# Performance work log

Measured on AMD Instinct MI355X. Metric: run time of the kernel, lower is better.

The kernel has to match this reference:

```python
import jax, jax.numpy as jnp
import numpy as np

B, S, D_IN, D_H = 4, 2048, 1024, 1024

def setup_inputs() -> dict:
    key = jax.random.key(0)
    kx, kq, kk, kv = jax.random.split(key, 4)
    # nn.Linear default init: U(-1/sqrt(fan_in), 1/sqrt(fan_in)); stored as [out, in]
    bound = 1.0 / np.sqrt(D_IN)
    x = jax.random.normal(kx, (B, S, D_IN), dtype=jnp.float32)
    W_q = jax.random.uniform(kq, (D_H, D_IN), jnp.float32, -bound, bound)
    W_k = jax.random.uniform(kk, (D_H, D_IN), jnp.float32, -bound, bound)
    W_v = jax.random.uniform(kv, (D_H, D_IN), jnp.float32, -bound, bound)
    return {"x": x, "W_q": W_q, "W_k": W_k, "W_v": W_v}

def reference(x, W_q, W_k, W_v):
    # Q = x @ W_q.T, etc. (nn.Linear with bias=False)
    Q = jnp.einsum('bsd,hd->bsh', x, W_q)
    K = jnp.einsum('bsd,hd->bsh', x, W_k)
    V = jnp.einsum('bsd,hd->bsh', x, W_v)
    # NOTE: original scales by sqrt(Q.shape[1]) == sqrt(seq_len), not sqrt(d)
    scale = 1.0 / jnp.sqrt(jnp.asarray(Q.shape[1], Q.dtype))
    scores = jnp.einsum('bqh,bkh->bqk', Q, K) * scale  # [B,S,S]
    attn = jax.nn.softmax(scores, axis=-1)
    return jnp.einsum('bqk,bkh->bqh', attn, V)
```

## Files before the change

kernel.cpp:

```cpp
#include <hip/hip_runtime.h>

typedef unsigned short ushort_t;
typedef __attribute__((ext_vector_type(8))) __bf16 bf16x8;
typedef __attribute__((ext_vector_type(4))) float floatx4;

__device__ __forceinline__ ushort_t f2bf(float f) {
    unsigned int u = __builtin_bit_cast(unsigned int, f);
    u = (u + 0x7fffu + ((u >> 16) & 1u)) >> 16;
    return (ushort_t)u;
}

__device__ __forceinline__ void async16(const ushort_t* g, ushort_t* l) {
    __builtin_amdgcn_global_load_lds(
        (const __attribute__((address_space(1))) unsigned int*)g,
        (__attribute__((address_space(3))) unsigned int*)l,
        16 , 0 , 0 );
}

__device__ __forceinline__ int sw(int row, int cg) {
    return ((row << 2) + ((cg ^ row ^ (row >> 2)) & 3)) << 3;
}

__device__ __forceinline__ int xcd_swz(int bid, int cpx) {
    return (bid & 7) * cpx + (bid >> 3);
}

template <int N>
__device__ __forceinline__ void vwait() {
    if constexpr (N == 0)      asm volatile("s_waitcnt vmcnt(0)" ::: "memory");
    else if constexpr (N == 3) asm volatile("s_waitcnt vmcnt(3)" ::: "memory");
    else if constexpr (N == 4) asm volatile("s_waitcnt vmcnt(4)" ::: "memory");
    else if constexpr (N == 6) asm volatile("s_waitcnt vmcnt(6)" ::: "memory");
    else if constexpr (N == 8) asm volatile("s_waitcnt vmcnt(8)" ::: "memory");
    else static_assert(N == 0, "unsupported vmcnt");
}

template <int BM, int BN, int IM, int IN, int NW, int NS>
__device__ __forceinline__ void gemm_core_p(
    const ushort_t* __restrict__ A, int lda,
    const ushort_t* __restrict__ B, int ldb,
    int K, int tile_m, int tile_n,
    ushort_t* buf,
    floatx4 (&acc)[IM][IN]) {

    constexpr int NT = NW * 64;
    constexpr int SA = BM * 4 / NT;
    constexpr int SB = BN * 4 / NT;
    constexpr int Q  = SA + SB;
    constexpr int SLOT = (BM + BN) * 32;
    constexpr int BOFF = BM * 32;

    const int tid  = threadIdx.x;
    const int lane = tid & 63;
    const int wave = tid >> 6;
    const int wm   = wave >> 1, wn = wave & 1;
    const int quad = lane >> 4;
    const int l16  = lane & 15;

#pragma unroll
    for (int i = 0; i < IM; i++)
#pragma unroll
        for (int j = 0; j < IN; j++) acc[i][j] = (floatx4){0.f, 0.f, 0.f, 0.f};

    const ushort_t* ga[SA];
    int la[SA];
#pragma unroll
    for (int s = 0; s < SA; s++) {
        int seg = tid + s * NT;
        int r = seg >> 2, c = (seg ^ r ^ (r >> 2)) & 3;
        ga[s] = A + (long)(r + tile_m) * lda + c * 8;
        la[s] = seg * 8;
    }
    const ushort_t* gb[SB];
    int lb[SB];
#pragma unroll
    for (int s = 0; s < SB; s++) {
        int seg = tid + s * NT;
        int r = seg >> 2, c = (seg ^ r ^ (r >> 2)) & 3;
        gb[s] = B + (long)(r + tile_n) * ldb + c * 8;
        lb[s] = BOFF + seg * 8;
    }

    const int nk = K >> 5;

#pragma unroll
    for (int p = 0; p < NS - 1; ++p) {
#pragma unroll
        for (int s = 0; s < SA; s++) async16(ga[s] + p * 32, buf + p * SLOT + la[s]);
#pragma unroll
        for (int s = 0; s < SB; s++) async16(gb[s] + p * 32, buf + p * SLOT + lb[s]);
    }

    int slot = 0, slot2 = NS - 1;
    for (int k = 0; k < nk; ++k) {
        const int rem = nk - 1 - k;
        if (rem >= NS - 2) {
            vwait<(NS - 2) * Q>();
        } else if (NS >= 4 && rem == 1) {
            vwait<Q>();
        } else {
            vwait<0>();
        }
        __builtin_amdgcn_s_barrier();
        asm volatile("" ::: "memory");

        if (k + NS - 1 < nk) {
            const int koff = (k + NS - 1) << 5;
            ushort_t* dst = buf + slot2 * SLOT;
#pragma unroll
            for (int s = 0; s < SA; s++) async16(ga[s] + koff, dst + la[s]);
#pragma unroll
            for (int s = 0; s < SB; s++) async16(gb[s] + koff, dst + lb[s]);
        }

        const ushort_t* as = buf + slot * SLOT;
        const ushort_t* bs = as + BOFF;
        bf16x8 af[IM], bfr[IN];
#pragma unroll
        for (int im = 0; im < IM; im++)
            af[im] = *(const bf16x8*)&as[sw(wm * IM * 16 + im * 16 + l16, quad)];
#pragma unroll
        for (int in = 0; in < IN; in++)
            bfr[in] = *(const bf16x8*)&bs[sw(wn * IN * 16 + in * 16 + l16, quad)];
#pragma unroll
        for (int im = 0; im < IM; im++)
#pragma unroll
            for (int in = 0; in < IN; in++)
                acc[im][in] = __builtin_amdgcn_mfma_f32_16x16x32_bf16(
                    af[im], bfr[in], acc[im][in], 0, 0, 0);

        slot  = (slot == NS - 1) ? 0 : slot + 1;
        slot2 = (slot2 == NS - 1) ? 0 : slot2 + 1;
    }
}

template <int MODE>
__device__ __forceinline__ void tile256_body(
    const ushort_t* __restrict__ sb,
    ushort_t* __restrict__ ldn,
    ushort_t* __restrict__ ldc,
    const ushort_t* __restrict__ gA, const ushort_t* __restrict__ gB,
    int lda, int ldb, int t,
    int rb0, int rb1, int abase, int bbase,
    floatx4 (&acc)[8][4]) {

    bf16x8 aR[4][2], bKc[2][2], bCc[2][2];

#pragma unroll
    for (int fr = 0; fr < 4; fr++) {
        aR[fr][0] = *(const bf16x8*)&sb[abase + fr * 1024 + rb0];
        aR[fr][1] = *(const bf16x8*)&sb[abase + fr * 1024 + rb1];
    }
#pragma unroll
    for (int fc = 0; fc < 2; fc++) {
        bKc[fc][0] = *(const bf16x8*)&sb[bbase + fc * 1024 + rb0];
        bKc[fc][1] = *(const bf16x8*)&sb[bbase + fc * 1024 + rb1];
    }
    if constexpr (MODE <= 1) {
        async16(gA + (long)128 * lda + (long)(t + 1) * 64, ldn + 8192);
        async16(gA + (long)192 * lda + (long)(t + 1) * 64, ldn + 12288);
    }
    asm volatile("s_waitcnt lgkmcnt(8)");
    __builtin_amdgcn_s_barrier();
    asm volatile("s_waitcnt lgkmcnt(0)");
    __builtin_amdgcn_s_setprio(1);
#pragma unroll
    for (int fr = 0; fr < 4; fr++)
#pragma unroll
        for (int fc = 0; fc < 2; fc++) {
            acc[fr][fc] = __builtin_amdgcn_mfma_f32_16x16x32_bf16(
                aR[fr][0], bKc[fc][0], acc[fr][fc], 0, 0, 0);
            acc[fr][fc] = __builtin_amdgcn_mfma_f32_16x16x32_bf16(
                aR[fr][1], bKc[fc][1], acc[fr][fc], 0, 0, 0);
        }
    __builtin_amdgcn_s_setprio(0);
    __builtin_amdgcn_s_barrier();

#pragma unroll
    for (int fc = 0; fc < 2; fc++) {
        bCc[fc][0] = *(const bf16x8*)&sb[bbase + (fc + 2) * 1024 + rb0];
        bCc[fc][1] = *(const bf16x8*)&sb[bbase + (fc + 2) * 1024 + rb1];
    }
    __builtin_amdgcn_s_barrier();
    asm volatile("s_waitcnt lgkmcnt(0)");
    __builtin_amdgcn_s_setprio(1);
#pragma unroll
    for (int fr = 0; fr < 4; fr++)
#pragma unroll
        for (int fc = 0; fc < 2; fc++) {
            acc[fr][fc + 2] = __builtin_amdgcn_mfma_f32_16x16x32_bf16(
                aR[fr][0], bCc[fc][0], acc[fr][fc + 2], 0, 0, 0);
            acc[fr][fc + 2] = __builtin_amdgcn_mfma_f32_16x16x32_bf16(
                aR[fr][1], bCc[fc][1], acc[fr][fc + 2], 0, 0, 0);
        }
    __builtin_amdgcn_s_setprio(0);
    __builtin_amdgcn_s_barrier();

#pragma unroll
    for (int fr = 0; fr < 4; fr++) {
        aR[fr][0] = *(const bf16x8*)&sb[abase + (fr + 4) * 1024 + rb0];
        aR[fr][1] = *(const bf16x8*)&sb[abase + (fr + 4) * 1024 + rb1];
    }
    if constexpr (MODE == 0) {
        async16(gB + (long)(t + 2) * 64,                  ldc + 16384);
        async16(gB + (long)64 * ldb + (long)(t + 2) * 64, ldc + 20480);
    }
    __builtin_amdgcn_s_barrier();
    asm volatile("s_waitcnt lgkmcnt(0)");
    __builtin_amdgcn_s_setprio(1);
#pragma unroll
    for (int fr = 0; fr < 4; fr++)
#pragma unroll
        for (int fc = 0; fc < 2; fc++) {
            acc[fr + 4][fc + 2] = __builtin_amdgcn_mfma_f32_16x16x32_bf16(
                aR[fr][0], bCc[fc][0], acc[fr + 4][fc + 2], 0, 0, 0);
            acc[fr + 4][fc + 2] = __builtin_amdgcn_mfma_f32_16x16x32_bf16(
                aR[fr][1], bCc[fc][1], acc[fr + 4][fc + 2], 0, 0, 0);
        }
    __builtin_amdgcn_s_setprio(0);
    __builtin_amdgcn_s_barrier();

    if constexpr (MODE == 0) {
        async16(gB + (long)128 * ldb + (long)(t + 2) * 64, ldc + 24576);
        async16(gB + (long)192 * ldb + (long)(t + 2) * 64, ldc + 28672);
        async16(gA + (long)(t + 2) * 64,                   ldc);
        async16(gA + (long)64 * lda + (long)(t + 2) * 64,  ldc + 4096);
    }
    __builtin_amdgcn_s_barrier();
    __builtin_amdgcn_s_setprio(1);
#pragma unroll
    for (int fr = 0; fr < 4; fr++)
#pragma unroll
        for (int fc = 0; fc < 2; fc++) {
            acc[fr + 4][fc] = __builtin_amdgcn_mfma_f32_16x16x32_bf16(
                aR[fr][0], bKc[fc][0], acc[fr + 4][fc], 0, 0, 0);
            acc[fr + 4][fc] = __builtin_amdgcn_mfma_f32_16x16x32_bf16(
                aR[fr][1], bKc[fc][1], acc[fr + 4][fc], 0, 0, 0);
        }
    __builtin_amdgcn_s_setprio(0);
    if constexpr (MODE == 0) asm volatile("s_waitcnt vmcnt(6)");
    else if constexpr (MODE == 1) asm volatile("s_waitcnt vmcnt(0)");
    __builtin_amdgcn_s_barrier();
}

__device__ __forceinline__ void gemm256_8ph(
    const ushort_t* __restrict__ A, int lda,
    const ushort_t* __restrict__ B, int ldb,
    int K, int tile_m, int tile_n,
    ushort_t* buf,
    floatx4 (&acc)[8][4]) {

    const int tid  = threadIdx.x;
    const int lane = tid & 63;
    const int wave = tid >> 6;
    const int wm   = wave >> 2;
    const int wn   = wave & 3;
    const int quad = lane >> 4;
    const int l16  = lane & 15;

#pragma unroll
    for (int i = 0; i < 8; i++)
#pragma unroll
        for (int j = 0; j < 4; j++) acc[i][j] = (floatx4){0.f, 0.f, 0.f, 0.f};

    const int srow = tid >> 3;
    const int scg  = (tid & 7) ^ (srow & 7);
    const ushort_t* gA = A + (long)(tile_m + srow) * lda + scg * 8;
    const ushort_t* gB = B + (long)(tile_n + srow) * ldb + scg * 8;
    ushort_t* const ld = buf + tid * 8;

    const int rb0 = l16 * 64 + (((quad)     ^ (l16 & 7)) << 3);
    const int rb1 = l16 * 64 + (((quad + 4) ^ (l16 & 7)) << 3);
    const int abase = wm * 8192;
    const int bbase = 16384 + (wn >> 1) * 8192 + (wn & 1) * 4096;

    const int nt = K >> 6;

    async16(gA,                    ld);
    async16(gA + (long)64 * lda,   ld + 4096);
    async16(gB,                    ld + 16384);
    async16(gB + (long)64 * ldb,   ld + 20480);
    async16(gB + (long)128 * ldb,  ld + 24576);
    async16(gB + (long)192 * ldb,  ld + 28672);
    async16(gA + (long)128 * lda,  ld + 8192);
    async16(gA + (long)192 * lda,  ld + 12288);
    async16(gB + 64,                   ld + 32768 + 16384);
    async16(gB + (long)64 * ldb + 64,  ld + 32768 + 20480);
    async16(gB + (long)128 * ldb + 64, ld + 32768 + 24576);
    async16(gB + (long)192 * ldb + 64, ld + 32768 + 28672);
    async16(gA + 64,                   ld + 32768);
    async16(gA + (long)64 * lda + 64,  ld + 32768 + 4096);
    asm volatile("s_waitcnt vmcnt(6)");
    __builtin_amdgcn_s_barrier();

    int t = 0;
#pragma unroll 1
    for (; t < nt - 2; ++t) {
        const int p = t & 1;
        tile256_body<0>(buf + p * 32768, ld + (p ^ 1) * 32768, ld + p * 32768,
                        gA, gB, lda, ldb, t, rb0, rb1, abase, bbase, acc);
    }
    {
        const int p = t & 1;
        tile256_body<1>(buf + p * 32768, ld + (p ^ 1) * 32768, ld + p * 32768,
                        gA, gB, lda, ldb, t, rb0, rb1, abase, bbase, acc);
        ++t;
    }
    {
        const int p = t & 1;
        tile256_body<2>(buf + p * 32768, ld + (p ^ 1) * 32768, ld + p * 32768,
                        gA, gB, lda, ldb, t, rb0, rb1, abase, bbase, acc);
    }
}

template <int MODE>
__device__ __forceinline__ void tile_bn256_body(
    const ushort_t* __restrict__ sb,
    ushort_t* __restrict__ ldn,
    ushort_t* __restrict__ ldc,
    const ushort_t* __restrict__ gA, const ushort_t* __restrict__ gB,
    int lda, int ldb, int t,
    int rb0, int rb1, int ab, int bb,
    floatx4 (&acc)[4][4]) {

    bf16x8 aR[4][2], bKc[2][2], bCc[2][2];

#pragma unroll
    for (int fr = 0; fr < 4; fr++) {
        aR[fr][0] = *(const bf16x8*)&sb[ab + fr * 1024 + rb0];
        aR[fr][1] = *(const bf16x8*)&sb[ab + fr * 1024 + rb1];
    }
#pragma unroll
    for (int fc = 0; fc < 2; fc++) {
        bKc[fc][0] = *(const bf16x8*)&sb[bb + fc * 4096 + rb0];
        bKc[fc][1] = *(const bf16x8*)&sb[bb + fc * 4096 + rb1];
    }
    if constexpr (MODE <= 1) {
        async16(gB + (long)128 * ldb + (long)(t + 1) * 64, ldn + 16384);
        async16(gB + (long)192 * ldb + (long)(t + 1) * 64, ldn + 20480);
    }
    asm volatile("s_waitcnt lgkmcnt(8)");
    __builtin_amdgcn_s_barrier();
    asm volatile("s_waitcnt lgkmcnt(0)");
    __builtin_amdgcn_s_setprio(1);
#pragma unroll
    for (int fr = 0; fr < 4; fr++)
#pragma unroll
        for (int fc = 0; fc < 2; fc++) {
            acc[fr][fc] = __builtin_amdgcn_mfma_f32_16x16x32_bf16(
                aR[fr][0], bKc[fc][0], acc[fr][fc], 0, 0, 0);
            acc[fr][fc] = __builtin_amdgcn_mfma_f32_16x16x32_bf16(
                aR[fr][1], bKc[fc][1], acc[fr][fc], 0, 0, 0);
        }
    __builtin_amdgcn_s_setprio(0);
    if constexpr (MODE <= 1) asm volatile("s_waitcnt vmcnt(6)");
    else                     asm volatile("s_waitcnt vmcnt(0)");
    __builtin_amdgcn_s_barrier();

#pragma unroll
    for (int fc = 0; fc < 2; fc++) {
        bCc[fc][0] = *(const bf16x8*)&sb[bb + (fc + 2) * 4096 + rb0];
        bCc[fc][1] = *(const bf16x8*)&sb[bb + (fc + 2) * 4096 + rb1];
    }
    if constexpr (MODE == 0) {
        async16(gA + (long)(t + 2) * 64,                  ldc);
        async16(gA + (long)64 * lda + (long)(t + 2) * 64, ldc + 4096);
        async16(gB + (long)(t + 2) * 64,                  ldc + 8192);
        async16(gB + (long)64 * ldb + (long)(t + 2) * 64, ldc + 12288);
    }
    __builtin_amdgcn_s_barrier();
    asm volatile("s_waitcnt lgkmcnt(0)");
    __builtin_amdgcn_s_setprio(1);
#pragma unroll
    for (int fr = 0; fr < 4; fr++)
#pragma unroll
        for (int fc = 0; fc < 2; fc++) {
            acc[fr][fc + 2] = __builtin_amdgcn_mfma_f32_16x16x32_bf16(
                aR[fr][0], bCc[fc][0], acc[fr][fc + 2], 0, 0, 0);
            acc[fr][fc + 2] = __builtin_amdgcn_mfma_f32_16x16x32_bf16(
                aR[fr][1], bCc[fc][1], acc[fr][fc + 2], 0, 0, 0);
        }
    __builtin_amdgcn_s_setprio(0);
    if constexpr (MODE == 0)      asm volatile("s_waitcnt vmcnt(6)");
    else if constexpr (MODE == 1) asm volatile("s_waitcnt vmcnt(2)");
    __builtin_amdgcn_s_barrier();
}

__device__ __forceinline__ void gemm_bn256_2ph(
    const ushort_t* __restrict__ A, int lda,
    const ushort_t* __restrict__ B, int ldb,
    int K, int tile_m, int tile_n,
    ushort_t* buf,
    floatx4 (&acc)[4][4]) {

    const int tid  = threadIdx.x;
    const int lane = tid & 63;
    const int wave = tid >> 6;
    const int wm   = wave >> 2;
    const int wn   = wave & 3;
    const int quad = lane >> 4;
    const int l16  = lane & 15;

#pragma unroll
    for (int i = 0; i < 4; i++)
#pragma unroll
        for (int j = 0; j < 4; j++) acc[i][j] = (floatx4){0.f, 0.f, 0.f, 0.f};

    const int srow = tid >> 3;
    const int scg  = (tid & 7) ^ (srow & 7);
    const ushort_t* gA = A + (long)(tile_m + srow) * lda + scg * 8;
    const ushort_t* gB = B + (long)(tile_n + srow) * ldb + scg * 8;
    ushort_t* const ld = buf + tid * 8;

    const int rb0 = l16 * 64 + (((quad)     ^ (l16 & 7)) << 3);
    const int rb1 = l16 * 64 + (((quad + 4) ^ (l16 & 7)) << 3);
    const int ab = wm * 4096;
    const int bb = 8192 + wn * 1024;

    const int nt = K >> 6;

    async16(gA,                    ld);
    async16(gA + (long)64 * lda,   ld + 4096);
    async16(gB,                    ld + 8192);
    async16(gB + (long)64 * ldb,   ld + 12288);
    async16(gB + (long)128 * ldb,  ld + 16384);
    async16(gB + (long)192 * ldb,  ld + 20480);
    async16(gA + 64,                   ld + 24576);
    async16(gA + (long)64 * lda + 64,  ld + 24576 + 4096);
    async16(gB + 64,                   ld + 24576 + 8192);
    async16(gB + (long)64 * ldb + 64,  ld + 24576 + 12288);
    asm volatile("s_waitcnt vmcnt(4)");
    __builtin_amdgcn_s_barrier();

    int t = 0;
#pragma unroll 1
    for (; t < nt - 2; ++t) {
        const int p = t & 1;
        tile_bn256_body<0>(buf + p * 24576, ld + (p ^ 1) * 24576, ld + p * 24576,
                           gA, gB, lda, ldb, t, rb0, rb1, ab, bb, acc);
    }
    {
        const int p = t & 1;
        tile_bn256_body<1>(buf + p * 24576, ld + (p ^ 1) * 24576, ld + p * 24576,
                           gA, gB, lda, ldb, t, rb0, rb1, ab, bb, acc);
        ++t;
    }
    {
        const int p = t & 1;
        tile_bn256_body<2>(buf + p * 24576, ld + (p ^ 1) * 24576, ld + p * 24576,
                           gA, gB, lda, ldb, t, rb0, rb1, ab, bb, acc);
    }
}

__global__ void prep_kernel(const float* __restrict__ x,
                            const float* __restrict__ wq,
                            const float* __restrict__ wk,
                            const float* __restrict__ wv,
                            ushort_t* __restrict__ xb,
                            ushort_t* __restrict__ wvb,
                            ushort_t* __restrict__ wqT,
                            ushort_t* __restrict__ wkT,
                            float* __restrict__ lsum) {
    const int bx = blockIdx.x;
    const int t = threadIdx.x;
    if (bx < 9216) {
        const float* src;
        ushort_t* dst;
        long g;
        if (bx < 8192) { src = x;  dst = xb;  g = ((long)bx * 256 + t) * 4; }
        else           { src = wv; dst = wvb; g = ((long)(bx - 8192) * 256 + t) * 4; }
        float4 v = *(const float4*)(src + g);
        ushort4 o;
        o.x = f2bf(v.x); o.y = f2bf(v.y); o.z = f2bf(v.z); o.w = f2bf(v.w);
        *(ushort4*)(dst + g) = o;
        return;
    }
    if (bx < 9224) {
        int idx = (bx - 9216) * 256 + t;
        ((float4*)lsum)[idx] = (float4){0.f, 0.f, 0.f, 0.f};
        return;
    }
    const int tt = bx - 9224;
    const float* src = (tt >= 256) ? wk : wq;
    ushort_t* dst = (tt >= 256) ? wkT : wqT;
    const int id = tt & 255;
    const int h0 = (id >> 4) * 64, d0 = (id & 15) * 64;
    __shared__ ushort_t tile[64 * 80];
    {
        int i = t >> 2, cg = (t & 3) << 4;
        const float4* p = (const float4*)(src + (long)(h0 + i) * 1024 + d0 + cg);
#pragma unroll
        for (int k = 0; k < 4; k++) {
            float4 v = p[k];
            ushort_t* q = &tile[i * 80 + cg + k * 4];
            q[0] = f2bf(v.x); q[1] = f2bf(v.y); q[2] = f2bf(v.z); q[3] = f2bf(v.w);
        }
    }
    __syncthreads();
    {
        int j = t >> 2, ig = (t & 3) << 4;
        ushort_t tmp[16];
#pragma unroll
        for (int k = 0; k < 16; k++) tmp[k] = tile[(ig + k) * 80 + j];
        ushort_t* o = dst + (long)(d0 + j) * 1024 + h0 + ig;
        *(uint4*)o = ((uint4*)tmp)[0];
        *(uint4*)(o + 8) = ((uint4*)tmp)[1];
    }
}

__global__ __launch_bounds__(512, 4) void gv_kernel(
    const ushort_t* __restrict__ wkT, const ushort_t* __restrict__ wqT,
    const ushort_t* __restrict__ wvb, const ushort_t* __restrict__ xb,
    ushort_t* __restrict__ Gb, ushort_t* __restrict__ VTb) {

    __shared__ __align__(16) ushort_t buf[3 * 384 * 32];

    const ushort_t *A, *B;
    ushort_t* C;
    int ldc, tile_m, tile_n;
    if (blockIdx.x < 32) {
        A = wkT; B = wqT; C = Gb; ldc = 1024;
        tile_m = (blockIdx.x >> 3) * 256;
        tile_n = (blockIdx.x & 7) * 128;
    } else {
        int id = blockIdx.x - 32;
        A = wvb; B = xb; C = VTb; ldc = 8192;
        tile_m = (id >> 6) * 256;
        tile_n = (id & 63) * 128;
    }

    floatx4 acc[4][4];
    gemm_core_p<256, 128, 4, 4, 8, 3>(A, 1024, B, 1024, 1024, tile_m, tile_n, buf, acc);

    const int lane = threadIdx.x & 63, wave = threadIdx.x >> 6;
    const int wm = wave >> 1, wn = wave & 1, quad = lane >> 4, l16 = lane & 15;
#pragma unroll
    for (int im = 0; im < 4; im++)
#pragma unroll
        for (int r = 0; r < 4; r++) {
            int row = tile_m + wm * 64 + im * 16 + quad * 4 + r;
#pragma unroll
            for (int in = 0; in < 4; in++) {
                int col = tile_n + wn * 64 + in * 16 + l16;
                C[(long)row * ldc + col] = f2bf(acc[im][in][r]);
            }
        }
}

__global__ __launch_bounds__(512, 2) void y_kernel(
    const ushort_t* __restrict__ xb,
    const ushort_t* __restrict__ Gb,
    ushort_t* __restrict__ Yb) {

    __shared__ __align__(16) ushort_t buf[49152];
    const int lin = xcd_swz(blockIdx.x, 32);
    const int tile_m = (lin >> 2) * 128;
    const int tile_n = (lin & 3) * 256;

    floatx4 acc[4][4];
    gemm_bn256_2ph(xb, 1024, Gb, 1024, 1024, tile_m, tile_n, buf, acc);

    const int lane = threadIdx.x & 63, wave = threadIdx.x >> 6;
    const int wm = wave >> 2, wn = wave & 3, quad = lane >> 4, l16 = lane & 15;
#pragma unroll
    for (int fr = 0; fr < 4; fr++)
#pragma unroll
        for (int r = 0; r < 4; r++) {
            int row = tile_m + wm * 64 + fr * 16 + quad * 4 + r;
#pragma unroll
            for (int fc = 0; fc < 4; fc++) {
                int col = tile_n + fc * 64 + wn * 16 + l16;
                Yb[(long)row * 1024 + col] = f2bf(acc[fr][fc][r]);
            }
        }
}

__global__ __launch_bounds__(512, 2) void pexp_kernel(
    const ushort_t* __restrict__ Yb,
    const ushort_t* __restrict__ xb,
    ushort_t* __restrict__ Pb,
    float* __restrict__ lsum) {

    __shared__ __align__(16) ushort_t buf[65536];

    const int lin = xcd_swz(blockIdx.x, 32);
    const int z = lin >> 6;
    const int tile_m = ((lin >> 3) & 7) * 256;
    const int tile_n = (lin & 7) * 256;

    const ushort_t* A = Yb + (long)z * 2097152;
    const ushort_t* B = xb + (long)z * 2097152;
    ushort_t* C = Pb + (long)z * 4194304;
    float* l = lsum + z * 2048;

    floatx4 acc[8][4];
    gemm256_8ph(A, 1024, B, 1024, 1024, tile_m, tile_n, buf, acc);

    const float scale = 0.022097086912079608f;
    const int lane = threadIdx.x & 63, wave = threadIdx.x >> 6;
    const int wm = wave >> 2, wn = wave & 3, quad = lane >> 4, l16 = lane & 15;
#pragma unroll
    for (int fr = 0; fr < 8; fr++)
#pragma unroll
        for (int rr = 0; rr < 4; rr++) {
            int row = tile_m + wm * 128 + fr * 16 + quad * 4 + rr;
            float psum = 0.f;
#pragma unroll
            for (int fc = 0; fc < 4; fc++) {
                int col = tile_n + wn * 64 + fc * 16 + l16;
                float e = __expf(acc[fr][fc][rr] * scale);
                C[(long)row * 2048 + col] = f2bf(e);
                psum += e;
            }
            psum += __shfl_xor(psum, 1, 64);
            psum += __shfl_xor(psum, 2, 64);
            psum += __shfl_xor(psum, 4, 64);
            psum += __shfl_xor(psum, 8, 64);
            if (l16 == 0) atomicAdd(&l[row], psum);
        }
}

__global__ __launch_bounds__(512, 2) void out_kernel(
    const ushort_t* __restrict__ Pb,
    const ushort_t* __restrict__ VTb,
    float* __restrict__ out,
    const float* __restrict__ lsum) {

    __shared__ __align__(16) ushort_t buf[49152];

    const int lin = xcd_swz(blockIdx.x, 32);
    const int z = lin >> 6;
    const int tile_m = ((lin >> 2) & 15) * 128;
    const int tile_n = (lin & 3) * 256;

    const ushort_t* A = Pb + (long)z * 4194304;
    const ushort_t* B = VTb + (long)z * 2048;
    float* C = out + (long)z * 2097152;
    const float* l = lsum + z * 2048;

    floatx4 acc[4][4];
    gemm_bn256_2ph(A, 2048, B, 8192, 2048, tile_m, tile_n, buf, acc);

    const int lane = threadIdx.x & 63, wave = threadIdx.x >> 6;
    const int wm = wave >> 2, wn = wave & 3, quad = lane >> 4, l16 = lane & 15;
#pragma unroll
    for (int fr = 0; fr < 4; fr++)
#pragma unroll
        for (int r = 0; r < 4; r++) {
            int row = tile_m + wm * 64 + fr * 16 + quad * 4 + r;
            float li = 1.0f / l[row];
#pragma unroll
            for (int fc = 0; fc < 4; fc++) {
                int col = tile_n + fc * 64 + wn * 16 + l16;
                C[(long)row * 1024 + col] = acc[fr][fc][r] * li;
            }
        }
}

extern "C" void kernel_launch(void* const* d_in, const int* in_sizes, int n_in,
                              void* d_out, int out_size, void* d_ws, size_t ws_size,
                              hipStream_t stream) {
    const float* x  = (const float*)d_in[0];
    const float* wq = (const float*)d_in[1];
    const float* wk = (const float*)d_in[2];
    const float* wv = (const float*)d_in[3];

    ushort_t* xb  = (ushort_t*)d_ws;
    ushort_t* wvb = xb  + 8388608;
    ushort_t* wqT = wvb + 1048576;
    ushort_t* wkT = wqT + 1048576;
    ushort_t* Gb  = wkT + 1048576;
    ushort_t* Yb  = Gb  + 1048576;
    ushort_t* VTb = Yb  + 8388608;
    ushort_t* Pb  = VTb + 8388608;
    float*    lsum = (float*)(Pb + 16777216);
    float*    out  = (float*)d_out;

    prep_kernel<<<9736, 256, 0, stream>>>(x, wq, wk, wv, xb, wvb, wqT, wkT, lsum);
    gv_kernel<<<288, 512, 0, stream>>>(wkT, wqT, wvb, xb, Gb, VTb);
    y_kernel<<<256, 512, 0, stream>>>(xb, Gb, Yb);
    pexp_kernel<<<256, 512, 0, stream>>>(Yb, xb, Pb, lsum);
    out_kernel<<<256, 512, 0, stream>>>(Pb, VTb, out, lsum);
}
```

Before: 229.1 us.

## Replace GEMM pipelines with one-barrier-per-tile prefetch schedules

```diff
diff --git a/kernel.cpp b/kernel.cpp
--- a/kernel.cpp
+++ b/kernel.cpp
@@ -17,152 +17,43 @@
         16 , 0 , 0 );
 }
 
-__device__ __forceinline__ int sw(int row, int cg) {
-    return ((row << 2) + ((cg ^ row ^ (row >> 2)) & 3)) << 3;
-}
-
 __device__ __forceinline__ int xcd_swz(int bid, int cpx) {
     return (bid & 7) * cpx + (bid >> 3);
 }
 
-template <int N>
-__device__ __forceinline__ void vwait() {
-    if constexpr (N == 0)      asm volatile("s_waitcnt vmcnt(0)" ::: "memory");
-    else if constexpr (N == 3) asm volatile("s_waitcnt vmcnt(3)" ::: "memory");
-    else if constexpr (N == 4) asm volatile("s_waitcnt vmcnt(4)" ::: "memory");
-    else if constexpr (N == 6) asm volatile("s_waitcnt vmcnt(6)" ::: "memory");
-    else if constexpr (N == 8) asm volatile("s_waitcnt vmcnt(8)" ::: "memory");
-    else static_assert(N == 0, "unsupported vmcnt");
-}
-
-template <int BM, int BN, int IM, int IN, int NW, int NS>
-__device__ __forceinline__ void gemm_core_p(
-    const ushort_t* __restrict__ A, int lda,
-    const ushort_t* __restrict__ B, int ldb,
-    int K, int tile_m, int tile_n,
-    ushort_t* buf,
-    floatx4 (&acc)[IM][IN]) {
-
-    constexpr int NT = NW * 64;
-    constexpr int SA = BM * 4 / NT;
-    constexpr int SB = BN * 4 / NT;
-    constexpr int Q  = SA + SB;
-    constexpr int SLOT = (BM + BN) * 32;
-    constexpr int BOFF = BM * 32;
-
-    const int tid  = threadIdx.x;
-    const int lane = tid & 63;
-    const int wave = tid >> 6;
-    const int wm   = wave >> 1, wn = wave & 1;
-    const int quad = lane >> 4;
-    const int l16  = lane & 15;
-
-#pragma unroll
-    for (int i = 0; i < IM; i++)
-#pragma unroll
-        for (int j = 0; j < IN; j++) acc[i][j] = (floatx4){0.f, 0.f, 0.f, 0.f};
-
-    const ushort_t* ga[SA];
-    int la[SA];
-#pragma unroll
-    for (int s = 0; s < SA; s++) {
-        int seg = tid + s * NT;
-        int r = seg >> 2, c = (seg ^ r ^ (r >> 2)) & 3;
-        ga[s] = A + (long)(r + tile_m) * lda + c * 8;
-        la[s] = seg * 8;
-    }
-    const ushort_t* gb[SB];
-    int lb[SB];
-#pragma unroll
-    for (int s = 0; s < SB; s++) {
-        int seg = tid + s * NT;
-        int r = seg >> 2, c = (seg ^ r ^ (r >> 2)) & 3;
-        gb[s] = B + (long)(r + tile_n) * ldb + c * 8;
-        lb[s] = BOFF + seg * 8;
-    }
-
-    const int nk = K >> 5;
-
-#pragma unroll
-    for (int p = 0; p < NS - 1; ++p) {
-#pragma unroll
-        for (int s = 0; s < SA; s++) async16(ga[s] + p * 32, buf + p * SLOT + la[s]);
-#pragma unroll
-        for (int s = 0; s < SB; s++) async16(gb[s] + p * 32, buf + p * SLOT + lb[s]);
-    }
-
-    int slot = 0, slot2 = NS - 1;
-    for (int k = 0; k < nk; ++k) {
-        const int rem = nk - 1 - k;
-        if (rem >= NS - 2) {
-            vwait<(NS - 2) * Q>();
-        } else if (NS >= 4 && rem == 1) {
-            vwait<Q>();
-        } else {
-            vwait<0>();
-        }
-        __builtin_amdgcn_s_barrier();
-        asm volatile("" ::: "memory");
-
-        if (k + NS - 1 < nk) {
-            const int koff = (k + NS - 1) << 5;
-            ushort_t* dst = buf + slot2 * SLOT;
-#pragma unroll
-            for (int s = 0; s < SA; s++) async16(ga[s] + koff, dst + la[s]);
-#pragma unroll
-            for (int s = 0; s < SB; s++) async16(gb[s] + koff, dst + lb[s]);
-        }
-
-        const ushort_t* as = buf + slot * SLOT;
-        const ushort_t* bs = as + BOFF;
-        bf16x8 af[IM], bfr[IN];
-#pragma unroll
-        for (int im = 0; im < IM; im++)
-            af[im] = *(const bf16x8*)&as[sw(wm * IM * 16 + im * 16 + l16, quad)];
-#pragma unroll
-        for (int in = 0; in < IN; in++)
-            bfr[in] = *(const bf16x8*)&bs[sw(wn * IN * 16 + in * 16 + l16, quad)];
-#pragma unroll
-        for (int im = 0; im < IM; im++)
-#pragma unroll
-            for (int in = 0; in < IN; in++)
-                acc[im][in] = __builtin_amdgcn_mfma_f32_16x16x32_bf16(
-                    af[im], bfr[in], acc[im][in], 0, 0, 0);
-
-        slot  = (slot == NS - 1) ? 0 : slot + 1;
-        slot2 = (slot2 == NS - 1) ? 0 : slot2 + 1;
-    }
-}
 
 template <int MODE>
-__device__ __forceinline__ void tile256_body(
-    const ushort_t* __restrict__ sb,
-    ushort_t* __restrict__ ldn,
-    ushort_t* __restrict__ ldc,
+__device__ __forceinline__ void frbn_tile(
+    const ushort_t* __restrict__ sb, ushort_t* __restrict__ dst,
     const ushort_t* __restrict__ gA, const ushort_t* __restrict__ gB,
-    int lda, int ldb, int t,
-    int rb0, int rb1, int abase, int bbase,
-    floatx4 (&acc)[8][4]) {
+    int lda, int ldb, long koff,
+    int rb0, int rb1, int ab, int bb,
+    floatx4 (&acc)[4][4]) {
+
+    if constexpr (MODE == 2) asm volatile("s_waitcnt vmcnt(0)");
+    else                     asm volatile("s_waitcnt vmcnt(6)");
+    __builtin_amdgcn_s_barrier();
+
+    if constexpr (MODE == 0) {
+        async16(gA + koff,                   dst);
+        async16(gA + (long)64 * lda + koff,  dst + 4096);
+        async16(gB + koff,                   dst + 8192);
+        async16(gB + (long)64 * ldb + koff,  dst + 12288);
+        async16(gB + (long)128 * ldb + koff, dst + 16384);
+        async16(gB + (long)192 * ldb + koff, dst + 20480);
+    }
 
     bf16x8 aR[4][2], bKc[2][2], bCc[2][2];
-
 #pragma unroll
     for (int fr = 0; fr < 4; fr++) {
-        aR[fr][0] = *(const bf16x8*)&sb[abase + fr * 1024 + rb0];
-        aR[fr][1] = *(const bf16x8*)&sb[abase + fr * 1024 + rb1];
+        aR[fr][0] = *(const bf16x8*)&sb[ab + fr * 1024 + rb0];
+        aR[fr][1] = *(const bf16x8*)&sb[ab + fr * 1024 + rb1];
     }
 #pragma unroll
     for (int fc = 0; fc < 2; fc++) {
-        bKc[fc][0] = *(const bf16x8*)&sb[bbase + fc * 1024 + rb0];
-        bKc[fc][1] = *(const bf16x8*)&sb[bbase + fc * 1024 + rb1];
-    }
-    if constexpr (MODE <= 1) {
-        async16(gA + (long)128 * lda + (long)(t + 1) * 64, ldn + 8192);
-        async16(gA + (long)192 * lda + (long)(t + 1) * 64, ldn + 12288);
-    }
-    asm volatile("s_waitcnt lgkmcnt(8)");
-    __builtin_amdgcn_s_barrier();
-    asm volatile("s_waitcnt lgkmcnt(0)");
+        bKc[fc][0] = *(const bf16x8*)&sb[bb + fc * 4096 + rb0];
+        bKc[fc][1] = *(const bf16x8*)&sb[bb + fc * 4096 + rb1];
+    }
     __builtin_amdgcn_s_setprio(1);
 #pragma unroll
     for (int fr = 0; fr < 4; fr++)
@@ -174,15 +65,12 @@
                 aR[fr][1], bKc[fc][1], acc[fr][fc], 0, 0, 0);
         }
     __builtin_amdgcn_s_setprio(0);
-    __builtin_amdgcn_s_barrier();
 
 #pragma unroll
     for (int fc = 0; fc < 2; fc++) {
-        bCc[fc][0] = *(const bf16x8*)&sb[bbase + (fc + 2) * 1024 + rb0];
-        bCc[fc][1] = *(const bf16x8*)&sb[bbase + (fc + 2) * 1024 + rb1];
-    }
-    __builtin_amdgcn_s_barrier();
-    asm volatile("s_waitcnt lgkmcnt(0)");
+        bCc[fc][0] = *(const bf16x8*)&sb[bb + (fc + 2) * 4096 + rb0];
+        bCc[fc][1] = *(const bf16x8*)&sb[bb + (fc + 2) * 4096 + rb1];
+    }
     __builtin_amdgcn_s_setprio(1);
 #pragma unroll
     for (int fr = 0; fr < 4; fr++)
@@ -194,61 +82,14 @@
                 aR[fr][1], bCc[fc][1], acc[fr][fc + 2], 0, 0, 0);
         }
     __builtin_amdgcn_s_setprio(0);
-    __builtin_amdgcn_s_barrier();
-
-#pragma unroll
-    for (int fr = 0; fr < 4; fr++) {
-        aR[fr][0] = *(const bf16x8*)&sb[abase + (fr + 4) * 1024 + rb0];
-        aR[fr][1] = *(const bf16x8*)&sb[abase + (fr + 4) * 1024 + rb1];
-    }
-    if constexpr (MODE == 0) {
-        async16(gB + (long)(t + 2) * 64,                  ldc + 16384);
-        async16(gB + (long)64 * ldb + (long)(t + 2) * 64, ldc + 20480);
-    }
-    __builtin_amdgcn_s_barrier();
-    asm volatile("s_waitcnt lgkmcnt(0)");
-    __builtin_amdgcn_s_setprio(1);
-#pragma unroll
-    for (int fr = 0; fr < 4; fr++)
-#pragma unroll
-        for (int fc = 0; fc < 2; fc++) {
-            acc[fr + 4][fc + 2] = __builtin_amdgcn_mfma_f32_16x16x32_bf16(
-                aR[fr][0], bCc[fc][0], acc[fr + 4][fc + 2], 0, 0, 0);
-            acc[fr + 4][fc + 2] = __builtin_amdgcn_mfma_f32_16x16x32_bf16(
-                aR[fr][1], bCc[fc][1], acc[fr + 4][fc + 2], 0, 0, 0);
-        }
-    __builtin_amdgcn_s_setprio(0);
-    __builtin_amdgcn_s_barrier();
-
-    if constexpr (MODE == 0) {
-        async16(gB + (long)128 * ldb + (long)(t + 2) * 64, ldc + 24576);
-        async16(gB + (long)192 * ldb + (long)(t + 2) * 64, ldc + 28672);
-        async16(gA + (long)(t + 2) * 64,                   ldc);
-        async16(gA + (long)64 * lda + (long)(t + 2) * 64,  ldc + 4096);
-    }
-    __builtin_amdgcn_s_barrier();
-    __builtin_amdgcn_s_setprio(1);
-#pragma unroll
-    for (int fr = 0; fr < 4; fr++)
-#pragma unroll
-        for (int fc = 0; fc < 2; fc++) {
-            acc[fr + 4][fc] = __builtin_amdgcn_mfma_f32_16x16x32_bf16(
-                aR[fr][0], bKc[fc][0], acc[fr + 4][fc], 0, 0, 0);
-            acc[fr + 4][fc] = __builtin_amdgcn_mfma_f32_16x16x32_bf16(
-                aR[fr][1], bKc[fc][1], acc[fr + 4][fc], 0, 0, 0);
-        }
-    __builtin_amdgcn_s_setprio(0);
-    if constexpr (MODE == 0) asm volatile("s_waitcnt vmcnt(6)");
-    else if constexpr (MODE == 1) asm volatile("s_waitcnt vmcnt(0)");
-    __builtin_amdgcn_s_barrier();
-}
-
-__device__ __forceinline__ void gemm256_8ph(
+}
+
+__device__ __forceinline__ void gemm_frbn(
     const ushort_t* __restrict__ A, int lda,
     const ushort_t* __restrict__ B, int ldb,
     int K, int tile_m, int tile_n,
     ushort_t* buf,
-    floatx4 (&acc)[8][4]) {
+    floatx4 (&acc)[4][4]) {
 
     const int tid  = threadIdx.x;
     const int lane = tid & 63;
@@ -259,7 +100,7 @@
     const int l16  = lane & 15;
 
 #pragma unroll
-    for (int i = 0; i < 8; i++)
+    for (int i = 0; i < 4; i++)
 #pragma unroll
         for (int j = 0; j < 4; j++) acc[i][j] = (floatx4){0.f, 0.f, 0.f, 0.f};
 
@@ -271,77 +112,75 @@
 
     const int rb0 = l16 * 64 + (((quad)     ^ (l16 & 7)) << 3);
     const int rb1 = l16 * 64 + (((quad + 4) ^ (l16 & 7)) << 3);
-    const int abase = wm * 8192;
-    const int bbase = 16384 + (wn >> 1) * 8192 + (wn & 1) * 4096;
+    const int ab = wm * 4096;
+    const int bb = 8192 + wn * 1024;
 
     const int nt = K >> 6;
 
-    async16(gA,                    ld);
-    async16(gA + (long)64 * lda,   ld + 4096);
-    async16(gB,                    ld + 16384);
-    async16(gB + (long)64 * ldb,   ld + 20480);
-    async16(gB + (long)128 * ldb,  ld + 24576);
-    async16(gB + (long)192 * ldb,  ld + 28672);
-    async16(gA + (long)128 * lda,  ld + 8192);
-    async16(gA + (long)192 * lda,  ld + 12288);
-    async16(gB + 64,                   ld + 32768 + 16384);
-    async16(gB + (long)64 * ldb + 64,  ld + 32768 + 20480);
-    async16(gB + (long)128 * ldb + 64, ld + 32768 + 24576);
-    async16(gB + (long)192 * ldb + 64, ld + 32768 + 28672);
-    async16(gA + 64,                   ld + 32768);
-    async16(gA + (long)64 * lda + 64,  ld + 32768 + 4096);
-    asm volatile("s_waitcnt vmcnt(6)");
-    __builtin_amdgcn_s_barrier();
-
+    async16(gA,                        ld);
+    async16(gA + (long)64 * lda,       ld + 4096);
+    async16(gB,                        ld + 8192);
+    async16(gB + (long)64 * ldb,       ld + 12288);
+    async16(gB + (long)128 * ldb,      ld + 16384);
+    async16(gB + (long)192 * ldb,      ld + 20480);
+    async16(gA + 64,                   ld + 24576);
+    async16(gA + (long)64 * lda + 64,  ld + 24576 + 4096);
+    async16(gB + 64,                   ld + 24576 + 8192);
+    async16(gB + (long)64 * ldb + 64,  ld + 24576 + 12288);
+    async16(gB + (long)128 * ldb + 64, ld + 24576 + 16384);
+    async16(gB + (long)192 * ldb + 64, ld + 24576 + 20480);
+
+    int cur = 0;
     int t = 0;
 #pragma unroll 1
     for (; t < nt - 2; ++t) {
-        const int p = t & 1;
-        tile256_body<0>(buf + p * 32768, ld + (p ^ 1) * 32768, ld + p * 32768,
-                        gA, gB, lda, ldb, t, rb0, rb1, abase, bbase, acc);
-    }
-    {
-        const int p = t & 1;
-        tile256_body<1>(buf + p * 32768, ld + (p ^ 1) * 32768, ld + p * 32768,
-                        gA, gB, lda, ldb, t, rb0, rb1, abase, bbase, acc);
-        ++t;
-    }
-    {
-        const int p = t & 1;
-        tile256_body<2>(buf + p * 32768, ld + (p ^ 1) * 32768, ld + p * 32768,
-                        gA, gB, lda, ldb, t, rb0, rb1, abase, bbase, acc);
-    }
+        const int nx = (cur == 0) ? 2 : cur - 1;
+        frbn_tile<0>(buf + cur * 24576, ld + nx * 24576,
+                     gA, gB, lda, ldb, (long)(t + 2) * 64,
+                     rb0, rb1, ab, bb, acc);
+        cur = (cur == 2) ? 0 : cur + 1;
+    }
+    frbn_tile<1>(buf + cur * 24576, ld, gA, gB, lda, ldb, 0,
+                 rb0, rb1, ab, bb, acc);
+    cur = (cur == 2) ? 0 : cur + 1;
+    frbn_tile<2>(buf + cur * 24576, ld, gA, gB, lda, ldb, 0,
+                 rb0, rb1, ab, bb, acc);
 }
 
 template <int MODE>
-__device__ __forceinline__ void tile_bn256_body(
-    const ushort_t* __restrict__ sb,
-    ushort_t* __restrict__ ldn,
-    ushort_t* __restrict__ ldc,
+__device__ __forceinline__ void fr256_tile(
+    const ushort_t* __restrict__ sb, ushort_t* __restrict__ dst,
     const ushort_t* __restrict__ gA, const ushort_t* __restrict__ gB,
-    int lda, int ldb, int t,
-    int rb0, int rb1, int ab, int bb,
-    floatx4 (&acc)[4][4]) {
+    int lda, int ldb, long koff,
+    int rb0, int rb1, int abase, int bbase,
+    floatx4 (&acc)[8][4]) {
+
+    asm volatile("s_waitcnt vmcnt(0)");
+    __builtin_amdgcn_s_barrier();
+
+    if constexpr (MODE == 0) {
+        async16(gA + koff,                   dst);
+        async16(gA + (long)64 * lda + koff,  dst + 4096);
+        async16(gA + (long)128 * lda + koff, dst + 8192);
+        async16(gA + (long)192 * lda + koff, dst + 12288);
+        async16(gB + koff,                   dst + 16384);
+        async16(gB + (long)64 * ldb + koff,  dst + 20480);
+        async16(gB + (long)128 * ldb + koff, dst + 24576);
+        async16(gB + (long)192 * ldb + koff, dst + 28672);
+    }
 
     bf16x8 aR[4][2], bKc[2][2], bCc[2][2];
 
 #pragma unroll
     for (int fr = 0; fr < 4; fr++) {
-        aR[fr][0] = *(const bf16x8*)&sb[ab + fr * 1024 + rb0];
-        aR[fr][1] = *(const bf16x8*)&sb[ab + fr * 1024 + rb1];
+        aR[fr][0] = *(const bf16x8*)&sb[abase + fr * 1024 + rb0];
+        aR[fr][1] = *(const bf16x8*)&sb[abase + fr * 1024 + rb1];
     }
 #pragma unroll
     for (int fc = 0; fc < 2; fc++) {
-        bKc[fc][0] = *(const bf16x8*)&sb[bb + fc * 4096 + rb0];
-        bKc[fc][1] = *(const bf16x8*)&sb[bb + fc * 4096 + rb1];
-    }
-    if constexpr (MODE <= 1) {
-        async16(gB + (long)128 * ldb + (long)(t + 1) * 64, ldn + 16384);
-        async16(gB + (long)192 * ldb + (long)(t + 1) * 64, ldn + 20480);
-    }
-    asm volatile("s_waitcnt lgkmcnt(8)");
-    __builtin_amdgcn_s_barrier();
-    asm volatile("s_waitcnt lgkmcnt(0)");
+        bKc[fc][0] = *(const bf16x8*)&sb[bbase + fc * 1024 + rb0];
+        bKc[fc][1] = *(const bf16x8*)&sb[bbase + fc * 1024 + rb1];
+    }
     __builtin_amdgcn_s_setprio(1);
 #pragma unroll
     for (int fr = 0; fr < 4; fr++)
@@ -353,23 +192,12 @@
                 aR[fr][1], bKc[fc][1], acc[fr][fc], 0, 0, 0);
         }
     __builtin_amdgcn_s_setprio(0);
-    if constexpr (MODE <= 1) asm volatile("s_waitcnt vmcnt(6)");
-    else                     asm volatile("s_waitcnt vmcnt(0)");
-    __builtin_amdgcn_s_barrier();
 
 #pragma unroll
     for (int fc = 0; fc < 2; fc++) {
-        bCc[fc][0] = *(const bf16x8*)&sb[bb + (fc + 2) * 4096 + rb0];
-        bCc[fc][1] = *(const bf16x8*)&sb[bb + (fc + 2) * 4096 + rb1];
-    }
-    if constexpr (MODE == 0) {
-        async16(gA + (long)(t + 2) * 64,                  ldc);
-        async16(gA + (long)64 * lda + (long)(t + 2) * 64, ldc + 4096);
-        async16(gB + (long)(t + 2) * 64,                  ldc + 8192);
-        async16(gB + (long)64 * ldb + (long)(t + 2) * 64, ldc + 12288);
-    }
-    __builtin_amdgcn_s_barrier();
-    asm volatile("s_waitcnt lgkmcnt(0)");
+        bCc[fc][0] = *(const bf16x8*)&sb[bbase + (fc + 2) * 1024 + rb0];
+        bCc[fc][1] = *(const bf16x8*)&sb[bbase + (fc + 2) * 1024 + rb1];
+    }
     __builtin_amdgcn_s_setprio(1);
 #pragma unroll
     for (int fr = 0; fr < 4; fr++)
@@ -381,17 +209,43 @@
                 aR[fr][1], bCc[fc][1], acc[fr][fc + 2], 0, 0, 0);
         }
     __builtin_amdgcn_s_setprio(0);
-    if constexpr (MODE == 0)      asm volatile("s_waitcnt vmcnt(6)");
-    else if constexpr (MODE == 1) asm volatile("s_waitcnt vmcnt(2)");
-    __builtin_amdgcn_s_barrier();
-}
-
-__device__ __forceinline__ void gemm_bn256_2ph(
+
+#pragma unroll
+    for (int fr = 0; fr < 4; fr++) {
+        aR[fr][0] = *(const bf16x8*)&sb[abase + (fr + 4) * 1024 + rb0];
+        aR[fr][1] = *(const bf16x8*)&sb[abase + (fr + 4) * 1024 + rb1];
+    }
+    __builtin_amdgcn_s_setprio(1);
+#pragma unroll
+    for (int fr = 0; fr < 4; fr++)
+#pragma unroll
+        for (int fc = 0; fc < 2; fc++) {
+            acc[fr + 4][fc + 2] = __builtin_amdgcn_mfma_f32_16x16x32_bf16(
+                aR[fr][0], bCc[fc][0], acc[fr + 4][fc + 2], 0, 0, 0);
+            acc[fr + 4][fc + 2] = __builtin_amdgcn_mfma_f32_16x16x32_bf16(
+                aR[fr][1], bCc[fc][1], acc[fr + 4][fc + 2], 0, 0, 0);
+        }
+    __builtin_amdgcn_s_setprio(0);
+
+    __builtin_amdgcn_s_setprio(1);
+#pragma unroll
+    for (int fr = 0; fr < 4; fr++)
+#pragma unroll
+        for (int fc = 0; fc < 2; fc++) {
+            acc[fr + 4][fc] = __builtin_amdgcn_mfma_f32_16x16x32_bf16(
+                aR[fr][0], bKc[fc][0], acc[fr + 4][fc], 0, 0, 0);
+            acc[fr + 4][fc] = __builtin_amdgcn_mfma_f32_16x16x32_bf16(
+                aR[fr][1], bKc[fc][1], acc[fr + 4][fc], 0, 0, 0);
+        }
+    __builtin_amdgcn_s_setprio(0);
+}
+
+__device__ __forceinline__ void gemm_fr256(
     const ushort_t* __restrict__ A, int lda,
     const ushort_t* __restrict__ B, int ldb,
     int K, int tile_m, int tile_n,
     ushort_t* buf,
-    floatx4 (&acc)[4][4]) {
+    floatx4 (&acc)[8][4]) {
 
     const int tid  = threadIdx.x;
     const int lane = tid & 63;
@@ -402,7 +256,7 @@
     const int l16  = lane & 15;
 
 #pragma unroll
-    for (int i = 0; i < 4; i++)
+    for (int i = 0; i < 8; i++)
 #pragma unroll
         for (int j = 0; j < 4; j++) acc[i][j] = (floatx4){0.f, 0.f, 0.f, 0.f};
 
@@ -414,41 +268,33 @@
 
     const int rb0 = l16 * 64 + (((quad)     ^ (l16 & 7)) << 3);
     const int rb1 = l16 * 64 + (((quad + 4) ^ (l16 & 7)) << 3);
-    const int ab = wm * 4096;
-    const int bb = 8192 + wn * 1024;
+    const int abase = wm * 8192;
+    const int bbase = 16384 + (wn >> 1) * 8192 + (wn & 1) * 4096;
 
     const int nt = K >> 6;
 
-    async16(gA,                    ld);
-    async16(gA + (long)64 * lda,   ld + 4096);
-    async16(gB,                    ld + 8192);
-    async16(gB + (long)64 * ldb,   ld + 12288);
-    async16(gB + (long)128 * ldb,  ld + 16384);
-    async16(gB + (long)192 * ldb,  ld + 20480);
-    async16(gA + 64,                   ld + 24576);
-    async16(gA + (long)64 * lda + 64,  ld + 24576 + 4096);
-    async16(gB + 64,                   ld + 24576 + 8192);
-    async16(gB + (long)64 * ldb + 64,  ld + 24576 + 12288);
-    asm volatile("s_waitcnt vmcnt(4)");
-    __builtin_amdgcn_s_barrier();
+    async16(gA,                   ld);
+    async16(gA + (long)64 * lda,  ld + 4096);
+    async16(gA + (long)128 * lda, ld + 8192);
+    async16(gA + (long)192 * lda, ld + 12288);
+    async16(gB,                   ld + 16384);
+    async16(gB + (long)64 * ldb,  ld + 20480);
+    async16(gB + (long)128 * ldb, ld + 24576);
+    async16(gB + (long)192 * ldb, ld + 28672);
 
     int t = 0;
 #pragma unroll 1
-    for (; t < nt - 2; ++t) {
+    for (; t < nt - 1; ++t) {
         const int p = t & 1;
-        tile_bn256_body<0>(buf + p * 24576, ld + (p ^ 1) * 24576, ld + p * 24576,
-                           gA, gB, lda, ldb, t, rb0, rb1, ab, bb, acc);
+        fr256_tile<0>(buf + p * 32768, ld + (p ^ 1) * 32768,
+                      gA, gB, lda, ldb, (long)(t + 1) * 64,
+                      rb0, rb1, abase, bbase, acc);
     }
     {
         const int p = t & 1;
-        tile_bn256_body<1>(buf + p * 24576, ld + (p ^ 1) * 24576, ld + p * 24576,
-                           gA, gB, lda, ldb, t, rb0, rb1, ab, bb, acc);
-        ++t;
-    }
-    {
-        const int p = t & 1;
-        tile_bn256_body<2>(buf + p * 24576, ld + (p ^ 1) * 24576, ld + p * 24576,
-                           gA, gB, lda, ldb, t, rb0, rb1, ab, bb, acc);
+        fr256_tile<1>(buf + p * 32768, ld,
+                      gA, gB, lda, ldb, 0,
+                      rb0, rb1, abase, bbase, acc);
     }
 }
 
@@ -508,41 +354,42 @@
     }
 }
 
-__global__ __launch_bounds__(512, 4) void gv_kernel(
+__global__ __launch_bounds__(512, 2) void gv_kernel(
     const ushort_t* __restrict__ wkT, const ushort_t* __restrict__ wqT,
     const ushort_t* __restrict__ wvb, const ushort_t* __restrict__ xb,
     ushort_t* __restrict__ Gb, ushort_t* __restrict__ VTb) {
 
-    __shared__ __align__(16) ushort_t buf[3 * 384 * 32];
-
+    __shared__ __align__(16) ushort_t buf[73728];
+
+    const int lin = xcd_swz(blockIdx.x, 36);
     const ushort_t *A, *B;
     ushort_t* C;
     int ldc, tile_m, tile_n;
-    if (blockIdx.x < 32) {
+    if (lin < 32) {
         A = wkT; B = wqT; C = Gb; ldc = 1024;
-        tile_m = (blockIdx.x >> 3) * 256;
-        tile_n = (blockIdx.x & 7) * 128;
+        tile_m = (lin >> 2) * 128;
+        tile_n = (lin & 3) * 256;
     } else {
-        int id = blockIdx.x - 32;
+        int id = lin - 32;
         A = wvb; B = xb; C = VTb; ldc = 8192;
-        tile_m = (id >> 6) * 256;
-        tile_n = (id & 63) * 128;
+        tile_m = (id >> 5) * 128;
+        tile_n = (id & 31) * 256;
     }
 
     floatx4 acc[4][4];
-    gemm_core_p<256, 128, 4, 4, 8, 3>(A, 1024, B, 1024, 1024, tile_m, tile_n, buf, acc);
+    gemm_frbn(A, 1024, B, 1024, 1024, tile_m, tile_n, buf, acc);
 
     const int lane = threadIdx.x & 63, wave = threadIdx.x >> 6;
-    const int wm = wave >> 1, wn = wave & 1, quad = lane >> 4, l16 = lane & 15;
-#pragma unroll
-    for (int im = 0; im < 4; im++)
+    const int wm = wave >> 2, wn = wave & 3, quad = lane >> 4, l16 = lane & 15;
+#pragma unroll
+    for (int fr = 0; fr < 4; fr++)
 #pragma unroll
         for (int r = 0; r < 4; r++) {
-            int row = tile_m + wm * 64 + im * 16 + quad * 4 + r;
-#pragma unroll
-            for (int in = 0; in < 4; in++) {
-                int col = tile_n + wn * 64 + in * 16 + l16;
-                C[(long)row * ldc + col] = f2bf(acc[im][in][r]);
+            int row = tile_m + wm * 64 + fr * 16 + quad * 4 + r;
+#pragma unroll
+            for (int fc = 0; fc < 4; fc++) {
+                int col = tile_n + fc * 64 + wn * 16 + l16;
+                C[(long)row * ldc + col] = f2bf(acc[fr][fc][r]);
             }
         }
 }
@@ -552,13 +399,13 @@
     const ushort_t* __restrict__ Gb,
     ushort_t* __restrict__ Yb) {
 
-    __shared__ __align__(16) ushort_t buf[49152];
+    __shared__ __align__(16) ushort_t buf[73728];
     const int lin = xcd_swz(blockIdx.x, 32);
     const int tile_m = (lin >> 2) * 128;
     const int tile_n = (lin & 3) * 256;
 
     floatx4 acc[4][4];
-    gemm_bn256_2ph(xb, 1024, Gb, 1024, 1024, tile_m, tile_n, buf, acc);
+    gemm_frbn(xb, 1024, Gb, 1024, 1024, tile_m, tile_n, buf, acc);
 
     const int lane = threadIdx.x & 63, wave = threadIdx.x >> 6;
     const int wm = wave >> 2, wn = wave & 3, quad = lane >> 4, l16 = lane & 15;
@@ -594,7 +441,7 @@
     float* l = lsum + z * 2048;
 
     floatx4 acc[8][4];
-    gemm256_8ph(A, 1024, B, 1024, 1024, tile_m, tile_n, buf, acc);
+    gemm_fr256(A, 1024, B, 1024, 1024, tile_m, tile_n, buf, acc);
 
     const float scale = 0.022097086912079608f;
     const int lane = threadIdx.x & 63, wave = threadIdx.x >> 6;
@@ -626,7 +473,7 @@
     float* __restrict__ out,
     const float* __restrict__ lsum) {
 
-    __shared__ __align__(16) ushort_t buf[49152];
+    __shared__ __align__(16) ushort_t buf[73728];
 
     const int lin = xcd_swz(blockIdx.x, 32);
     const int z = lin >> 6;
@@ -639,7 +486,7 @@
     const float* l = lsum + z * 2048;
 
     floatx4 acc[4][4];
-    gemm_bn256_2ph(A, 2048, B, 8192, 2048, tile_m, tile_n, buf, acc);
+    gemm_frbn(A, 2048, B, 8192, 2048, tile_m, tile_n, buf, acc);
 
     const int lane = threadIdx.x & 63, wave = threadIdx.x >> 6;
     const int wm = wave >> 2, wn = wave & 3, quad = lane >> 4, l16 = lane & 15;
```

Result: faster. 219.3 us (-4.3%).
